# Kernel tuning notes

Measured on AMD Instinct MI355X. Metric: run time of the kernel, lower is better.

Reference implementation:

```python
import jax, jax.numpy as jnp
import numpy as np

T, S, B, E, H = 1024, 1024, 4, 1024, 16
D = E // H
SCALE = D ** -0.5


def setup_inputs() -> dict:
    key = jax.random.key(0)
    ks = jax.random.split(key, 10)
    std = 0.02
    return {
        "q": jax.random.normal(ks[0], (T, B, E), jnp.float32),
        "k": jax.random.normal(ks[1], (S, B, E), jnp.float32),
        "v": jax.random.normal(ks[2], (S, B, E), jnp.float32),
        "Wq": jax.random.normal(ks[3], (E, E), jnp.float32) * std,
        "Wk": jax.random.normal(ks[4], (E, E), jnp.float32) * std,
        "Wv": jax.random.normal(ks[5], (E, E), jnp.float32) * std,
        "Wp": jax.random.normal(ks[6], (E, E), jnp.float32) * std,
        "bp": jnp.zeros((E,), jnp.float32),
        "attn_bias": jax.random.normal(ks[7], (B, H, T, S), jnp.float32) * std,
        "key_padding_mask": jax.random.bernoulli(ks[8], 0.1, (B, S)),
    }


def reference(q, k, v, Wq, Wk, Wv, Wp, bp, attn_bias, key_padding_mask):
    # projections (no bias: qkv_bias=False); torch Linear is x @ W.T
    qh = (q @ Wq.T).reshape(T, B, H, D).transpose(1, 2, 0, 3) * SCALE  # [B,H,T,D]
    kh = (k @ Wk.T).reshape(S, B, H, D).transpose(1, 2, 0, 3)          # [B,H,S,D]
    vh = (v @ Wv.T).reshape(S, B, H, D).transpose(1, 2, 0, 3)          # [B,H,S,D]

    scores = jnp.einsum("bhid,bhjd->bhij", qh, kh) + attn_bias        # [B,H,T,S]
    # detached max-subtract (as in original)
    scores = scores - jax.lax.stop_gradient(scores.max(axis=-1, keepdims=True))

    mask = key_padding_mask[:, None, None, :]                          # [B,1,1,S], True = masked
    neg = jnp.finfo(scores.dtype).min
    attn = jax.nn.softmax(jnp.where(mask, neg, scores), axis=-1)
    attn = jnp.where(mask, jnp.zeros((), scores.dtype), attn)          # XSoftmax: zero masked probs

    out = jnp.einsum("bhij,bhjd->bhid", attn, vh)                      # [B,H,T,D]
    out = out.transpose(2, 0, 1, 3).reshape(T, B, E)                   # [T,B,E]
    out = out @ Wp.T + bp                                              # output projection
    return (out, attn)
```

## Files before the change

kernel.cpp:

```cpp
#include <hip/hip_runtime.h>
#include <math.h>

constexpr int T_ = 1024, S_ = 1024, B_ = 4, E_ = 1024, H_ = 16, D_ = 64;
constexpr float SCALE_ = 0.125f;
constexpr size_t NH_ = (size_t)B_ * H_ * T_ * D_;
constexpr size_t EE_ = (size_t)E_ * E_;

typedef _Float16 h8 __attribute__((ext_vector_type(8)));
typedef _Float16 h4 __attribute__((ext_vector_type(4)));
typedef float f4 __attribute__((ext_vector_type(4)));

__device__ inline f4 mfma16(h8 a, h8 b, f4 c) {
    return __builtin_amdgcn_mfma_f32_16x16x32_f16(a, b, c, 0, 0, 0);
}

__device__ inline void gload_lds16(const void* g, void* l) {
    __builtin_amdgcn_global_load_lds(
        (const __attribute__((address_space(1))) void*)g,
        (__attribute__((address_space(3))) void*)l, 16, 0, 0);
}

__global__ __launch_bounds__(256) void cvt_all(
    const float* __restrict__ q, const float* __restrict__ k,
    const float* __restrict__ v, const float* __restrict__ wq,
    const float* __restrict__ wk, const float* __restrict__ wv,
    const float* __restrict__ wp, _Float16* __restrict__ dst)
{
    const int i8 = blockIdx.x * 256 + threadIdx.x;
    constexpr int BIG = (int)(NH_ / 8);
    constexpr int WSZ = (int)(EE_ / 8);
    const float* src;
    int loc;
    if (i8 < 3 * BIG) {
        int t = i8 / BIG; loc = i8 - t * BIG;
        src = t == 0 ? q : (t == 1 ? k : v);
    } else {
        int r = i8 - 3 * BIG;
        int t = r / WSZ; loc = r - t * WSZ;
        src = t == 0 ? wq : (t == 1 ? wk : (t == 2 ? wv : wp));
    }
    const float* p = src + (size_t)loc * 8;
    float4 a = *(const float4*)p;
    float4 b = *(const float4*)(p + 4);
    h8 o;
    o[0] = (_Float16)a.x; o[1] = (_Float16)a.y;
    o[2] = (_Float16)a.z; o[3] = (_Float16)a.w;
    o[4] = (_Float16)b.x; o[5] = (_Float16)b.y;
    o[6] = (_Float16)b.z; o[7] = (_Float16)b.w;
    *(h8*)&dst[(size_t)i8 * 8] = o;
}

template <typename EPI>
__device__ inline void gemm_core(
    const _Float16* __restrict__ A, const _Float16* __restrict__ W,
    int m0, int n0, EPI epi)
{
    __shared__ _Float16 As[64][64];
    __shared__ _Float16 Bs[128][64];

    const int tid = threadIdx.x;
    const int w = tid >> 6, l = tid & 63, lr = l & 15, lg = l >> 4;
    const int wr = w >> 2, wc = w & 3;

    const int srow = (w << 3) + (l >> 3);
    const int sg   = (l & 7) ^ (srow & 7);
    char* AsB = (char*)As;
    char* BsB = (char*)Bs;
    char* ldsA  = AsB + w * 1024;
    char* ldsB0 = BsB + w * 1024;
    char* ldsB1 = BsB + 8192 + w * 1024;

    f4 acc[2][2];
#pragma unroll
    for (int mi = 0; mi < 2; ++mi)
#pragma unroll
        for (int ni = 0; ni < 2; ++ni) acc[mi][ni] = (f4){0.f, 0.f, 0.f, 0.f};

    for (int k0 = 0; k0 < 1024; k0 += 64) {
        gload_lds16(&A[(size_t)(m0 + srow) * 1024 + k0 + sg * 8], ldsA);
        gload_lds16(&W[(size_t)(n0 + srow) * 1024 + k0 + sg * 8], ldsB0);
        gload_lds16(&W[(size_t)(n0 + 64 + srow) * 1024 + k0 + sg * 8], ldsB1);
        __syncthreads();
#pragma unroll
        for (int kk = 0; kk < 2; ++kk) {
            h8 af[2], bf[2];
#pragma unroll
            for (int mi = 0; mi < 2; ++mi) {
                int r = wr * 32 + mi * 16 + lr, kc = kk * 4 + lg;
                af[mi] = *(const h8*)(AsB + r * 128 + ((kc ^ (r & 7)) << 4));
            }
#pragma unroll
            for (int ni = 0; ni < 2; ++ni) {
                int r = wc * 32 + ni * 16 + lr, kc = kk * 4 + lg;
                bf[ni] = *(const h8*)(BsB + r * 128 + ((kc ^ (r & 7)) << 4));
            }
#pragma unroll
            for (int mi = 0; mi < 2; ++mi)
#pragma unroll
                for (int ni = 0; ni < 2; ++ni)
                    acc[mi][ni] = mfma16(af[mi], bf[ni], acc[mi][ni]);
        }
        __syncthreads();
    }

#pragma unroll
    for (int mi = 0; mi < 2; ++mi)
#pragma unroll
        for (int ni = 0; ni < 2; ++ni)
#pragma unroll
            for (int r = 0; r < 4; ++r) {
                int row = m0 + wr * 32 + mi * 16 + lg * 4 + r;
                int col = n0 + wc * 32 + ni * 16 + lr;
                epi(row, col, acc[mi][ni][r]);
            }
}

__global__ __launch_bounds__(512) void qkv_gemm(
    const _Float16* __restrict__ q16, const _Float16* __restrict__ k16,
    const _Float16* __restrict__ v16, const _Float16* __restrict__ Wq16,
    const _Float16* __restrict__ Wk16, const _Float16* __restrict__ Wv16,
    _Float16* __restrict__ qh, _Float16* __restrict__ kh,
    _Float16* __restrict__ vhT)
{
    const int z = blockIdx.z;
    const _Float16* A = z == 0 ? q16 : (z == 1 ? k16 : v16);
    const _Float16* W = z == 0 ? Wq16 : (z == 1 ? Wk16 : Wv16);
    _Float16* C = z == 0 ? qh : (z == 1 ? kh : vhT);
    const float scale = (z == 0) ? SCALE_ : 1.0f;
    const int m0 = blockIdx.x * 64, n0 = blockIdx.y * 128;

    if (z < 2) {
        gemm_core(A, W, m0, n0, [&](int row, int col, float vv) {
            int t = row >> 2, b = row & 3, h = col >> 6, d = col & 63;
            C[(((size_t)b * H_ + h) * T_ + t) * D_ + d] = (_Float16)(vv * scale);
        });
    } else {
        gemm_core(A, W, m0, n0, [&](int row, int col, float vv) {
            int s = row >> 2, b = row & 3, h = col >> 6, d = col & 63;
            C[(((size_t)b * H_ + h) * D_ + d) * S_ + s] = (_Float16)vv;
        });
    }
}

__global__ __launch_bounds__(512) void out_gemm(
    const _Float16* __restrict__ oh, const _Float16* __restrict__ Wp16,
    const float* __restrict__ bp, float* __restrict__ out)
{
    const int m0 = blockIdx.x * 64, n0 = blockIdx.y * 128;
    gemm_core(oh, Wp16, m0, n0, [&](int row, int col, float vv) {
        out[(size_t)row * E_ + col] = vv + bp[col];
    });
}

__global__ __launch_bounds__(512, 6) void fused_attn(
    const _Float16* __restrict__ qh, const _Float16* __restrict__ kh,
    const _Float16* __restrict__ vhT, const float* __restrict__ bias,
    const int* __restrict__ mask, float* __restrict__ attn,
    _Float16* __restrict__ oh)
{
    __shared__ _Float16 Pf[16 * 1024];
    __shared__ int aux_i[1024];
    __shared__ float sinv16[16];
    char* Pb = (char*)Pf;

    const int bid = blockIdx.x;
    const int vid = (bid & 7) * 512 + (bid >> 3);
    const int bh = vid >> 6;
    const int t0 = (vid & 63) * 16;
    const int b = bh >> 4, h = bh & 15;
    const int tid = threadIdx.x;
    const int w = tid >> 6, l = tid & 63, lr = l & 15, lg = l >> 4;

    const int rr2 = tid >> 5;
    const int c2  = tid & 31;
    const float* brow = bias + ((size_t)bh * T_ + t0 + rr2) * S_;
    f4 bv[8];
#pragma unroll
    for (int j = 0; j < 8; ++j)
        bv[j] = *(const f4*)&brow[c2 * 4 + j * 128];

    for (int i = tid; i < S_; i += 512) aux_i[i] = mask[(size_t)b * S_ + i];

    const _Float16* qbase = qh + ((size_t)bh * T_ + t0) * D_;
    h8 qf0 = *(const h8*)&qbase[(size_t)lr * D_ + lg * 8];
    h8 qf1 = *(const h8*)&qbase[(size_t)lr * D_ + 32 + lg * 8];

    const _Float16* kbase = kh + (size_t)bh * S_ * D_;
    const int wbase = w * 128;

    __syncthreads();

#pragma unroll
    for (int sub = 0; sub < 8; ++sub) {
        int s0 = wbase + sub * 16;
        h8 kf0 = *(const h8*)&kbase[(size_t)(s0 + lr) * D_ + lg * 8];
        h8 kf1 = *(const h8*)&kbase[(size_t)(s0 + lr) * D_ + 32 + lg * 8];
        f4 c = (f4){0.f, 0.f, 0.f, 0.f};
        c = mfma16(kf0, qf0, c);
        c = mfma16(kf1, qf1, c);
        int4 mv = *(const int4*)&aux_i[s0 + lg * 4];
        h4 pv;
        pv[0] = mv.x ? (_Float16)0.f : (_Float16)__expf(c[0]);
        pv[1] = mv.y ? (_Float16)0.f : (_Float16)__expf(c[1]);
        pv[2] = mv.z ? (_Float16)0.f : (_Float16)__expf(c[2]);
        pv[3] = mv.w ? (_Float16)0.f : (_Float16)__expf(c[3]);
        int off = (lr * 2048 + (s0 + lg * 4) * 2) ^ ((lr & 7) << 4);
        *(h4*)(Pb + off) = pv;
    }
    __syncthreads();

    {
        h4 p[8];
#pragma unroll
        for (int j = 0; j < 8; ++j) {
            int off = (rr2 * 2048 + (c2 * 4 + j * 128) * 2) ^ ((rr2 & 7) << 4);
            p[j] = *(const h4*)(Pb + off);
        }

        h4 pn[8];
        float rs = 0.f;
#pragma unroll
        for (int j = 0; j < 8; ++j) {
            float p0 = (float)p[j][0] * __expf(bv[j][0]);
            float p1 = (float)p[j][1] * __expf(bv[j][1]);
            float p2 = (float)p[j][2] * __expf(bv[j][2]);
            float p3 = (float)p[j][3] * __expf(bv[j][3]);
            rs += (p0 + p1) + (p2 + p3);
            pn[j][0] = (_Float16)p0; pn[j][1] = (_Float16)p1;
            pn[j][2] = (_Float16)p2; pn[j][3] = (_Float16)p3;
        }

        rs += __shfl_xor(rs, 1); rs += __shfl_xor(rs, 2);
        rs += __shfl_xor(rs, 4); rs += __shfl_xor(rs, 8);
        rs += __shfl_xor(rs, 16);
        float inv = 1.0f / rs;
        if (c2 == 0) sinv16[rr2] = inv;

#pragma unroll
        for (int j = 0; j < 8; ++j) {
            int off = (rr2 * 2048 + (c2 * 4 + j * 128) * 2) ^ ((rr2 & 7) << 4);
            *(h4*)(Pb + off) = pn[j];
        }
        float* arow = attn + ((size_t)bh * T_ + t0 + rr2) * S_;
#pragma unroll
        for (int j = 0; j < 8; ++j) {
            f4 o = {(float)pn[j][0] * inv, (float)pn[j][1] * inv,
                    (float)pn[j][2] * inv, (float)pn[j][3] * inv};
            __builtin_nontemporal_store(o, (f4*)&arow[c2 * 4 + j * 128]);
        }
    }
    __syncthreads();

    {
        const int sh = w & 1, dbase = (w >> 1) * 16;
        const _Float16* vbase = vhT + (size_t)bh * D_ * S_;
        f4 acc = (f4){0.f, 0.f, 0.f, 0.f};
#pragma unroll 4
        for (int kc = 0; kc < 16; ++kc) {
            int s0 = sh * 512 + kc * 32;
            int off = (lr * 2048 + (s0 + lg * 8) * 2) ^ ((lr & 7) << 4);
            h8 pf = *(const h8*)(Pb + off);
            h8 vf = *(const h8*)&vbase[(size_t)(dbase + lr) * S_ + s0 + lg * 8];
            acc = mfma16(pf, vf, acc);
        }
        float* pvred = (float*)aux_i;
        if (sh) {
#pragma unroll
            for (int r = 0; r < 4; ++r)
                pvred[(lg * 4 + r) * 64 + dbase + lr] = acc[r];
        }
        __syncthreads();
        if (!sh) {
#pragma unroll
            for (int r = 0; r < 4; ++r) {
                int t = lg * 4 + r;
                float o = (acc[r] + pvred[t * 64 + dbase + lr]) * sinv16[t];
                oh[((size_t)(t0 + t) * B_ + b) * E_ + h * 64 + dbase + lr] = (_Float16)o;
            }
        }
    }
}

extern "C" void kernel_launch(void* const* d_in, const int* in_sizes, int n_in,
                              void* d_out, int out_size, void* d_ws, size_t ws_size,
                              hipStream_t stream)
{
    const float* q    = (const float*)d_in[0];
    const float* k    = (const float*)d_in[1];
    const float* v    = (const float*)d_in[2];
    const float* Wq   = (const float*)d_in[3];
    const float* Wk   = (const float*)d_in[4];
    const float* Wv   = (const float*)d_in[5];
    const float* Wp   = (const float*)d_in[6];
    const float* bp   = (const float*)d_in[7];
    const float* bias = (const float*)d_in[8];
    const int*   mask = (const int*)d_in[9];

    float* out  = (float*)d_out;
    float* attn = out + (size_t)T_ * B_ * E_;

    _Float16* qh   = (_Float16*)d_ws;
    _Float16* kh   = qh + NH_;
    _Float16* vhT  = kh + NH_;
    _Float16* oh   = vhT + NH_;
    _Float16* q16  = oh + NH_;
    _Float16* k16  = q16 + NH_;
    _Float16* v16  = k16 + NH_;
    _Float16* Wq16 = v16 + NH_;
    _Float16* Wk16 = Wq16 + EE_;
    _Float16* Wv16 = Wk16 + EE_;
    _Float16* Wp16 = Wv16 + EE_;

    dim3 blk(512);

    cvt_all<<<dim3(8192), dim3(256), 0, stream>>>(q, k, v, Wq, Wk, Wv, Wp, q16);

    qkv_gemm<<<dim3(64, 8, 3), blk, 0, stream>>>(
        q16, k16, v16, Wq16, Wk16, Wv16, qh, kh, vhT);

    fused_attn<<<dim3(4096), blk, 0, stream>>>(qh, kh, vhT, bias, mask, attn, oh);

    out_gemm<<<dim3(64, 8), blk, 0, stream>>>(oh, Wp16, bp, out);
}
```

Measured before the change: 258.2 us.

## Fuse attention bias into score exponent via lane shuffles, drop LDS rewrite pass

Bias values are now loaded in an MFMA-friendly per-wave layout and redistributed with lane shuffles so that exp(score+bias) is computed directly in the QK loop. Row sums are accumulated there and reduced through a small shared array. This removes the second LDS read-modify-write pass over P and one block barrier before the PV stage. The PV loop unroll also goes from 4 to 8. The cost is extra shuffles and more register pressure in the QK loop. The score and bias are also now summed in fp32 before exponentiation, rather than multiplying two exps with the first rounded to fp16.

```diff
diff --git a/kernel.cpp b/kernel.cpp
--- a/kernel.cpp
+++ b/kernel.cpp
@@ -160,6 +160,7 @@
 {
     __shared__ _Float16 Pf[16 * 1024];
     __shared__ int aux_i[1024];
+    __shared__ float wsum[8][16];
     __shared__ float sinv16[16];
     char* Pb = (char*)Pf;
 
@@ -171,25 +172,26 @@
     const int tid = threadIdx.x;
     const int w = tid >> 6, l = tid & 63, lr = l & 15, lg = l >> 4;
 
-    const int rr2 = tid >> 5;
-    const int c2  = tid & 31;
-    const float* brow = bias + ((size_t)bh * T_ + t0 + rr2) * S_;
+    const float* bbase = bias + ((size_t)bh * T_ + t0) * S_;
+    const int brow_ = l >> 2, bq_ = l & 3;
     f4 bv[8];
 #pragma unroll
     for (int j = 0; j < 8; ++j)
-        bv[j] = *(const f4*)&brow[c2 * 4 + j * 128];
-
-    for (int i = tid; i < S_; i += 512) aux_i[i] = mask[(size_t)b * S_ + i];
+        bv[j] = *(const f4*)&bbase[(size_t)brow_ * S_ + w * 128 + j * 16 + bq_ * 4];
 
     const _Float16* qbase = qh + ((size_t)bh * T_ + t0) * D_;
     h8 qf0 = *(const h8*)&qbase[(size_t)lr * D_ + lg * 8];
     h8 qf1 = *(const h8*)&qbase[(size_t)lr * D_ + 32 + lg * 8];
+    __builtin_amdgcn_sched_barrier(0);
+
+    for (int i = tid; i < S_; i += 512) aux_i[i] = mask[(size_t)b * S_ + i];
+    __syncthreads();
 
     const _Float16* kbase = kh + (size_t)bh * S_ * D_;
     const int wbase = w * 128;
-
-    __syncthreads();
-
+    const int srcLane = lr * 4 + lg;
+
+    float rs = 0.f;
 #pragma unroll
     for (int sub = 0; sub < 8; ++sub) {
         int s0 = wbase + sub * 16;
@@ -198,64 +200,51 @@
         f4 c = (f4){0.f, 0.f, 0.f, 0.f};
         c = mfma16(kf0, qf0, c);
         c = mfma16(kf1, qf1, c);
+        float b0 = __shfl(bv[sub][0], srcLane);
+        float b1 = __shfl(bv[sub][1], srcLane);
+        float b2 = __shfl(bv[sub][2], srcLane);
+        float b3 = __shfl(bv[sub][3], srcLane);
         int4 mv = *(const int4*)&aux_i[s0 + lg * 4];
+        float p0 = mv.x ? 0.f : __expf(c[0] + b0);
+        float p1 = mv.y ? 0.f : __expf(c[1] + b1);
+        float p2 = mv.z ? 0.f : __expf(c[2] + b2);
+        float p3 = mv.w ? 0.f : __expf(c[3] + b3);
+        rs += (p0 + p1) + (p2 + p3);
         h4 pv;
-        pv[0] = mv.x ? (_Float16)0.f : (_Float16)__expf(c[0]);
-        pv[1] = mv.y ? (_Float16)0.f : (_Float16)__expf(c[1]);
-        pv[2] = mv.z ? (_Float16)0.f : (_Float16)__expf(c[2]);
-        pv[3] = mv.w ? (_Float16)0.f : (_Float16)__expf(c[3]);
+        pv[0] = (_Float16)p0; pv[1] = (_Float16)p1;
+        pv[2] = (_Float16)p2; pv[3] = (_Float16)p3;
         int off = (lr * 2048 + (s0 + lg * 4) * 2) ^ ((lr & 7) << 4);
         *(h4*)(Pb + off) = pv;
     }
+    rs += __shfl_xor(rs, 16); rs += __shfl_xor(rs, 32);
+    if (l < 16) wsum[w][lr] = rs;
     __syncthreads();
 
     {
-        h4 p[8];
+        const int rr2 = tid >> 5;
+        const int c2  = tid & 31;
+        float s8 = 0.f;
+#pragma unroll
+        for (int ww = 0; ww < 8; ++ww) s8 += wsum[ww][rr2];
+        float inv = 1.0f / s8;
+        if (c2 == 0) sinv16[rr2] = inv;
+        float* arow = attn + ((size_t)bh * T_ + t0 + rr2) * S_;
 #pragma unroll
         for (int j = 0; j < 8; ++j) {
-            int off = (rr2 * 2048 + (c2 * 4 + j * 128) * 2) ^ ((rr2 & 7) << 4);
-            p[j] = *(const h4*)(Pb + off);
-        }
-
-        h4 pn[8];
-        float rs = 0.f;
-#pragma unroll
-        for (int j = 0; j < 8; ++j) {
-            float p0 = (float)p[j][0] * __expf(bv[j][0]);
-            float p1 = (float)p[j][1] * __expf(bv[j][1]);
-            float p2 = (float)p[j][2] * __expf(bv[j][2]);
-            float p3 = (float)p[j][3] * __expf(bv[j][3]);
-            rs += (p0 + p1) + (p2 + p3);
-            pn[j][0] = (_Float16)p0; pn[j][1] = (_Float16)p1;
-            pn[j][2] = (_Float16)p2; pn[j][3] = (_Float16)p3;
-        }
-
-        rs += __shfl_xor(rs, 1); rs += __shfl_xor(rs, 2);
-        rs += __shfl_xor(rs, 4); rs += __shfl_xor(rs, 8);
-        rs += __shfl_xor(rs, 16);
-        float inv = 1.0f / rs;
-        if (c2 == 0) sinv16[rr2] = inv;
-
-#pragma unroll
-        for (int j = 0; j < 8; ++j) {
-            int off = (rr2 * 2048 + (c2 * 4 + j * 128) * 2) ^ ((rr2 & 7) << 4);
-            *(h4*)(Pb + off) = pn[j];
-        }
-        float* arow = attn + ((size_t)bh * T_ + t0 + rr2) * S_;
-#pragma unroll
-        for (int j = 0; j < 8; ++j) {
-            f4 o = {(float)pn[j][0] * inv, (float)pn[j][1] * inv,
-                    (float)pn[j][2] * inv, (float)pn[j][3] * inv};
-            __builtin_nontemporal_store(o, (f4*)&arow[c2 * 4 + j * 128]);
-        }
-    }
-    __syncthreads();
+            int col = c2 * 4 + j * 128;
+            int off = (rr2 * 2048 + col * 2) ^ ((rr2 & 7) << 4);
+            h4 p = *(const h4*)(Pb + off);
+            f4 o = {(float)p[0] * inv, (float)p[1] * inv,
+                    (float)p[2] * inv, (float)p[3] * inv};
+            __builtin_nontemporal_store(o, (f4*)&arow[col]);
+        }
+    }
 
     {
         const int sh = w & 1, dbase = (w >> 1) * 16;
         const _Float16* vbase = vhT + (size_t)bh * D_ * S_;
         f4 acc = (f4){0.f, 0.f, 0.f, 0.f};
-#pragma unroll 4
+#pragma unroll 8
         for (int kc = 0; kc < 16; ++kc) {
             int s0 = sh * 512 + kc * 32;
             int off = (lr * 2048 + (s0 + lg * 8) * 2) ^ ((lr & 7) << 4);
```

New measurement: 259.3 us. No clear change (+0.4%).
